# Kernel optimization log

Measured on AMD Instinct MI355X. Metric: run time of the kernel, lower is better.

The kernel has to match this reference:

```python
import jax, jax.numpy as jnp
import numpy as np

BS, S = 8, 1024
D_MODEL, N_HEADS, D_K = 256, 8, 32
H_SHARED, H_SEL = 2, 2
N_DYN = N_HEADS - H_SHARED
D_FF = 1024
N_BLOCKS = 2
L = 3 * N_BLOCKS  # blocks_1 (N_BLOCKS layers) + blocks_2 (2*N_BLOCKS layers)
NEG = -1e9


def _layernorm(x, g, b):
    m = x.mean(-1, keepdims=True)
    v = ((x - m) ** 2).mean(-1, keepdims=True)
    return (x - m) * jax.lax.rsqrt(v + 1e-5) * g + b


def _layer(p, mask_val, query, values, q4router, apply_pos):
    (Wq, bq, Wv, bv, Wg, Wo, bo, g1, be1, Wf1, bf1, Wf2, bf2, g2, be2) = p
    bs, s, dm = query.shape
    q = query @ Wq + bq            # kq_same=True -> k = q
    v = values @ Wv + bv
    qh = q.reshape(bs, s, N_HEADS, D_K).transpose(0, 2, 1, 3)   # [b,h,s,d]
    vh = v.reshape(bs, s, N_HEADS, D_K).transpose(0, 2, 1, 3)
    scores = jnp.einsum('bhqd,bhkd->bhqk', qh, qh) / (D_K ** 0.5)
    # nopeek = triu(ones,k=mask); allowed where nopeek==0 -> col < row + mask
    allowed = jnp.arange(s)[None, :] < (jnp.arange(s)[:, None] + mask_val)
    scores = jnp.where(allowed[None, None], scores, NEG)
    attnw = jax.nn.softmax(scores, axis=-1)
    # head routing: replicate torch view->permute->reshape order exactly
    qr = q4router.reshape(bs, s, N_HEADS, D_K).transpose(0, 2, 1, 3).reshape(bs * s, N_HEADS * D_K)
    gates = jax.nn.softmax(qr @ Wg, axis=1)                     # [bs*s, N_DYN]
    _, idx = jax.lax.top_k(gates, H_SEL)
    dyn_mask = jax.nn.one_hot(idx, N_DYN, dtype=gates.dtype).sum(axis=1)
    dyn_scores = gates * dyn_mask
    hs = dyn_mask.sum(axis=0)
    hp = gates.mean(axis=0)
    bal = ((hs / (hs.sum() + 1e-5)) * (hp / (hp.sum() + 1e-5))).sum()
    routing = jnp.concatenate(
        [jnp.ones((bs, s, H_SHARED), gates.dtype), dyn_scores.reshape(bs, s, N_DYN)], axis=-1)
    routing = routing.mean(axis=1)[:, :, None, None]            # [b,h,1,1]
    out = jnp.einsum('bhqk,bhkd->bhqd', attnw, vh) * routing
    out = out.transpose(0, 2, 1, 3).reshape(bs, s, dm) @ Wo + bo
    query = _layernorm(query + out, g1, be1)
    if apply_pos:
        ff = jax.nn.relu(query @ Wf1 + bf1) @ Wf2 + bf2
        query = _layernorm(query + ff, g2, be2)
    return query, bal


def _forward(q_embed_data, qa_embed_data, Wq, bq, Wv, bv, Wg, Wo, bo,
             ln1_w, ln1_b, Wf1, bf1, Wf2, bf2, ln2_w, ln2_b):
    stacks = (Wq, bq, Wv, bv, Wg, Wo, bo, ln1_w, ln1_b, Wf1, bf1, Wf2, bf2, ln2_w, ln2_b)
    params = [tuple(a[i] for a in stacks) for i in range(L)]
    x, y = q_embed_data, qa_embed_data
    for i in range(N_BLOCKS):
        y, _ = _layer(params[i], 1, y, y, x, True)
    attn = jnp.zeros((), jnp.float32)
    li = N_BLOCKS
    for _ in range(N_BLOCKS):
        x, _ = _layer(params[li], 1, x, x, x, False)  # self-block, no FFN
        li += 1
        x, attn = _layer(params[li], 0, x, y, x, True)  # cross to y, strict causal
        li += 1
    return x, attn


def setup_inputs():
    key = jax.random.key(0)
    ks = jax.random.split(key, 10)
    w = lambda k, shp: (jax.random.normal(k, shp, jnp.float32) * 0.02)
    return {
        'q_embed_data': jax.random.normal(ks[0], (BS, S, D_MODEL), jnp.float32),
        'qa_embed_data': jax.random.normal(ks[1], (BS, S, D_MODEL), jnp.float32),
        'Wq': w(ks[2], (L, D_MODEL, D_MODEL)), 'bq': jnp.zeros((L, D_MODEL), jnp.float32),
        'Wv': w(ks[3], (L, D_MODEL, D_MODEL)), 'bv': jnp.zeros((L, D_MODEL), jnp.float32),
        'Wg': w(ks[4], (L, D_MODEL, N_DYN)),
        'Wo': w(ks[5], (L, D_MODEL, D_MODEL)), 'bo': jnp.zeros((L, D_MODEL), jnp.float32),
        'ln1_w': jnp.ones((L, D_MODEL), jnp.float32), 'ln1_b': jnp.zeros((L, D_MODEL), jnp.float32),
        'Wf1': w(ks[6], (L, D_MODEL, D_FF)), 'bf1': jnp.zeros((L, D_FF), jnp.float32),
        'Wf2': w(ks[7], (L, D_FF, D_MODEL)), 'bf2': jnp.zeros((L, D_MODEL), jnp.float32),
        'ln2_w': jnp.ones((L, D_MODEL), jnp.float32), 'ln2_b': jnp.zeros((L, D_MODEL), jnp.float32),
    }


def reference(q_embed_data, qa_embed_data, Wq, bq, Wv, bv, Wg, Wo, bo,
              ln1_w, ln1_b, Wf1, bf1, Wf2, bf2, ln2_w, ln2_b):
    return _forward(q_embed_data, qa_embed_data, Wq, bq, Wv, bv, Wg, Wo, bo,
                    ln1_w, ln1_b, Wf1, bf1, Wf2, bf2, ln2_w, ln2_b)
```

## Files before the change

kernel.cpp:

```cpp
#include <hip/hip_runtime.h>


constexpr int DMODEL = 256;
constexpr int SEQ    = 1024;
constexpr int BATCH  = 8;
constexpr int NHEADS = 8;
constexpr int DKDIM  = 32;
constexpr int NDYN_C = 6;
constexpr int NTOK_C = BATCH * SEQ;
constexpr int DFF_C  = 1024;

using frag_bf16 = __attribute__((ext_vector_type(8))) short;
using f32x4    = __attribute__((ext_vector_type(4))) float;
typedef unsigned short ushort_t;

__device__ __forceinline__ ushort_t f2bf(float f) {
  unsigned u = __float_as_uint(f);
  unsigned r = (u + 0x7fffu + ((u >> 16) & 1u)) >> 16;
  return (ushort_t)r;
}

__device__ __forceinline__ unsigned cvt_pk_bf16(float lo, float hi) {
  unsigned r;
  asm("v_cvt_pk_bf16_f32 %0, %1, %2" : "=v"(r) : "v"(lo), "v"(hi));
  return r;
}

#define GLOAD_LDS16(gsrc, ldst)                                             \
  __builtin_amdgcn_global_load_lds(                                         \
      (const __attribute__((address_space(1))) void*)(gsrc),                \
      (__attribute__((address_space(3))) void*)(ldst), 16, 0, 0)

#define SYNC_DRAIN()                                                        \
  do {                                                                      \
    asm volatile("s_waitcnt vmcnt(0) lgkmcnt(0)" ::: "memory");             \
    __builtin_amdgcn_sched_barrier(0);                                      \
    __syncthreads();                                                        \
  } while (0)

template<int MODE>
__device__ __forceinline__
void gemm_body(int bx, int by,
               const ushort_t* __restrict__ A, const ushort_t* __restrict__ B,
               const float* __restrict__ bias, void* __restrict__ Cp,
               int M, int N, int K) {
  __shared__ ushort_t sA[2][4096];
  __shared__ ushort_t sB[2][4096];
  const int tid = threadIdx.x;
  const int wid = tid >> 6, lane = tid & 63;
  const int li = lane & 15, g = lane >> 4;
  const int wr = wid >> 1, wc = wid & 1;
  const int m0 = by * 64, n0 = bx * 64;
  f32x4 acc[2][2] = {};
  const int srow = wid * 8 + (lane >> 3);
  const int schk = (lane & 7) ^ (lane >> 3);
  const ushort_t* gA1 = &A[(size_t)(m0 + srow) * K + schk * 8];
  const ushort_t* gA2 = &A[(size_t)(m0 + 32 + srow) * K + schk * 8];
  const ushort_t* gB1 = &B[(size_t)(n0 + srow) * K + schk * 8];
  const ushort_t* gB2 = &B[(size_t)(n0 + 32 + srow) * K + schk * 8];
  const int nk = K >> 6;

  GLOAD_LDS16(gA1, sA[0] + wid * 512);
  GLOAD_LDS16(gA2, sA[0] + 2048 + wid * 512);
  GLOAD_LDS16(gB1, sB[0] + wid * 512);
  GLOAD_LDS16(gB2, sB[0] + 2048 + wid * 512);
  SYNC_DRAIN();

  auto compute = [&](int cur) {
#pragma unroll
    for (int s = 0; s < 2; ++s) {
      frag_bf16 af[2], bf[2];
#pragma unroll
      for (int m = 0; m < 2; ++m) {
        const int row = wr * 32 + m * 16 + li;
        af[m] = *reinterpret_cast<const frag_bf16*>(
            &sA[cur][row * 64 + ((s * 4 + g) ^ (row & 7)) * 8]);
      }
#pragma unroll
      for (int n = 0; n < 2; ++n) {
        const int row = wc * 32 + n * 16 + li;
        bf[n] = *reinterpret_cast<const frag_bf16*>(
            &sB[cur][row * 64 + ((s * 4 + g) ^ (row & 7)) * 8]);
      }
#pragma unroll
      for (int m = 0; m < 2; ++m)
#pragma unroll
        for (int n = 0; n < 2; ++n)
          acc[m][n] = __builtin_amdgcn_mfma_f32_16x16x32_bf16(af[m], bf[n], acc[m][n], 0, 0, 0);
    }
  };

  for (int kt = 0; kt < nk - 1; ++kt) {
    const int cur = kt & 1;
    const int k1 = (kt + 1) << 6;
    GLOAD_LDS16(gA1 + k1, sA[cur ^ 1] + wid * 512);
    GLOAD_LDS16(gA2 + k1, sA[cur ^ 1] + 2048 + wid * 512);
    GLOAD_LDS16(gB1 + k1, sB[cur ^ 1] + wid * 512);
    GLOAD_LDS16(gB2 + k1, sB[cur ^ 1] + 2048 + wid * 512);
    compute(cur);
    SYNC_DRAIN();
  }
  compute((nk - 1) & 1);

  constexpr float QSCALE = 0.42044820762685725f;
#pragma unroll
  for (int m = 0; m < 2; ++m)
#pragma unroll
    for (int n = 0; n < 2; ++n)
#pragma unroll
      for (int r = 0; r < 4; ++r) {
        const int mg = m0 + wr * 32 + m * 16 + g * 4 + r;
        const int ng = n0 + wc * 32 + n * 16 + li;
        if (MODE == 0) {
          ((float*)Cp)[(size_t)mg * N + ng] = acc[m][n][r] + bias[ng];
        } else if (MODE == 1) {
          ((ushort_t*)Cp)[(size_t)mg * N + ng] = f2bf((acc[m][n][r] + bias[ng]) * QSCALE);
        } else if (MODE == 2) {
          ((ushort_t*)Cp)[(size_t)mg * N + ng] = f2bf(fmaxf(acc[m][n][r] + bias[ng], 0.0f));
        } else {
          ((ushort_t*)Cp)[((size_t)((ng >> 10) * 256 + mg)) * SEQ + (ng & 1023)] =
              f2bf(acc[m][n][r] + bias[mg]);
        }
      }
}

template<int MODE>
__global__ __launch_bounds__(256)
void gemm_mfma_k(const ushort_t* __restrict__ A, const ushort_t* __restrict__ B,
                 const float* __restrict__ bias, void* __restrict__ Cp,
                 int M, int N, int K) {
  gemm_body<MODE>(blockIdx.x, blockIdx.y, A, B, bias, Cp, M, N, K);
}

__global__ __launch_bounds__(256)
void gemm_qv_k(const ushort_t* __restrict__ Aq, const ushort_t* __restrict__ Bq,
               const float* __restrict__ biasq, void* __restrict__ Cq,
               const ushort_t* __restrict__ Av, const ushort_t* __restrict__ Bv,
               const float* __restrict__ biasv, void* __restrict__ Cv) {
  if (blockIdx.z == 0)
    gemm_body<1>(blockIdx.y, blockIdx.x, Aq, Bq, biasq, Cq, NTOK_C, DMODEL, DMODEL);
  else
    gemm_body<3>(blockIdx.x, blockIdx.y, Av, Bv, biasv, Cv, DMODEL, NTOK_C, DMODEL);
}

__global__ __launch_bounds__(256)
void transpose_k(const float* __restrict__ in, ushort_t* __restrict__ out, int R, int C) {
  __shared__ float t[32][33];
  const int z = blockIdx.z;
  const int c0 = blockIdx.x * 32, r0 = blockIdx.y * 32;
  const int tx = threadIdx.x & 31, ty = threadIdx.x >> 5;
  const float* ip = in + (size_t)z * R * C;
  ushort_t* op = out + (size_t)z * R * C;
#pragma unroll
  for (int i = 0; i < 4; ++i) t[ty + 8 * i][tx] = ip[(size_t)(r0 + ty + 8 * i) * C + c0 + tx];
  __syncthreads();
#pragma unroll
  for (int i = 0; i < 4; ++i)
    op[(size_t)(c0 + ty + 8 * i) * R + r0 + tx] = f2bf(t[tx][ty + 8 * i]);
}

__global__ __launch_bounds__(256)
void conv_init_k(const float* __restrict__ src, float* __restrict__ dstF,
                 ushort_t* __restrict__ dstB) {
  const int i = blockIdx.x * 256 + threadIdx.x;
  const float4 v = reinterpret_cast<const float4*>(src)[i];
  reinterpret_cast<float4*>(dstF)[i] = v;
  ushort4 b;
  b.x = f2bf(v.x); b.y = f2bf(v.y); b.z = f2bf(v.z); b.w = f2bf(v.w);
  reinterpret_cast<ushort4*>(dstB)[i] = b;
}

__global__ __launch_bounds__(256)
void attn_mfma_k(const ushort_t* __restrict__ qb, const ushort_t* __restrict__ vbT,
                 const float* __restrict__ routing8, ushort_t* __restrict__ out,
                 int mask_val) {
  __shared__ ushort_t sk[2][2048];
  __shared__ ushort_t sv[2][2048];
  __shared__ ushort_t pbuf[4096];
  const int gid = blockIdx.x;
  const int b = gid & 7;
  const int slot = gid >> 3;
  const int h = (slot >> 4) & 7;
  const int qblk = 15 - (slot & 15);
  const int q0 = qblk * 64;
  const int tid = threadIdx.x;
  const int wave = tid >> 6, lane = tid & 63;
  const int g = lane >> 4, li = lane & 15;
  const int qw = q0 + wave * 16;
  const int qrow = qw + li;

  const frag_bf16 qf = *reinterpret_cast<const frag_bf16*>(
      &qb[((size_t)(b * SEQ + qrow)) * DMODEL + h * DKDIM + g * 8]);

  float mrun = -INFINITY, lrun = 0.f;
  f32x4 o0 = {0.f, 0.f, 0.f, 0.f}, o1 = {0.f, 0.f, 0.f, 0.f};
  ushort_t* pP = &pbuf[wave * 1024];

  const ushort_t* gK = &qb[((size_t)(b * SEQ + wave * 16 + li)) * DMODEL + h * DKDIM + g * 8];
  const ushort_t* gV = &vbT[((size_t)((b * NHEADS + h) * DKDIM) + wave * 8 + (lane >> 3)) * SEQ
                            + ((lane & 7) ^ (lane >> 3)) * 8];

  const int nt = qblk + 1;
  GLOAD_LDS16(gK, sk[0] + wave * 512);
  GLOAD_LDS16(gV, sv[0] + wave * 512);
  SYNC_DRAIN();

  auto tile_step = [&](int t, int cur) {
    const int kt = t * 64;
    f32x4 s[4];
#pragma unroll
    for (int kb = 0; kb < 4; ++kb) {
      frag_bf16 kf = *reinterpret_cast<const frag_bf16*>(&sk[cur][(kb * 64 + g * 16 + li) * 8]);
      f32x4 z = {0.f, 0.f, 0.f, 0.f};
      s[kb] = __builtin_amdgcn_mfma_f32_16x16x32_bf16(kf, qf, z, 0, 0, 0);
    }
    const bool need_mask = (kt + 63) >= (qw + mask_val);
    if (need_mask) {
#pragma unroll
      for (int kb = 0; kb < 4; ++kb)
#pragma unroll
        for (int r = 0; r < 4; ++r) {
          const int col = kt + kb * 16 + 4 * g + r;
          if (col >= (qrow + mask_val)) s[kb][r] = -1e9f;
        }
    }
    float tm = -INFINITY;
#pragma unroll
    for (int kb = 0; kb < 4; ++kb)
#pragma unroll
      for (int r = 0; r < 4; ++r) tm = fmaxf(tm, s[kb][r]);
    tm = fmaxf(tm, __shfl_xor(tm, 16, 64));
    tm = fmaxf(tm, __shfl_xor(tm, 32, 64));
    const float mnew = fmaxf(mrun, tm);
    const float scl = __expf(mrun - mnew);
    float p[4][4];
    float psum = 0.f;
#pragma unroll
    for (int kb = 0; kb < 4; ++kb)
#pragma unroll
      for (int r = 0; r < 4; ++r) { p[kb][r] = __expf(s[kb][r] - mnew); psum += p[kb][r]; }
    psum += __shfl_xor(psum, 16, 64);
    psum += __shfl_xor(psum, 32, 64);
    lrun = lrun * scl + psum;
    mrun = mnew;
#pragma unroll
    for (int r = 0; r < 4; ++r) { o0[r] *= scl; o1[r] *= scl; }
#pragma unroll
    for (int kb = 0; kb < 4; ++kb)
#pragma unroll
      for (int pair = 0; pair < 2; ++pair) {
        const unsigned pk = cvt_pk_bf16(p[kb][2 * pair], p[kb][2 * pair + 1]);
        const int addr = (((kb >> 1) * 4 + (kb & 1) * 2 + (g >> 1)) * 16 + li) * 8
                         + 4 * (g & 1) + 2 * pair;
        *reinterpret_cast<unsigned*>(&pP[addr]) = pk;
      }
    __threadfence_block();
#pragma unroll
    for (int c = 0; c < 2; ++c) {
      frag_bf16 pf = *reinterpret_cast<const frag_bf16*>(&pP[((c * 4 + g) * 16 + li) * 8]);
      frag_bf16 vf0 = *reinterpret_cast<const frag_bf16*>(
          &sv[cur][li * 64 + ((4 * c + g) ^ (li & 7)) * 8]);
      frag_bf16 vf1 = *reinterpret_cast<const frag_bf16*>(
          &sv[cur][(16 + li) * 64 + ((4 * c + g) ^ (li & 7)) * 8]);
      o0 = __builtin_amdgcn_mfma_f32_16x16x32_bf16(vf0, pf, o0, 0, 0, 0);
      o1 = __builtin_amdgcn_mfma_f32_16x16x32_bf16(vf1, pf, o1, 0, 0, 0);
    }
  };

  for (int t = 0; t < nt - 1; ++t) {
    const int cur = t & 1;
    const int kt = t * 64;
    GLOAD_LDS16(gK + (size_t)(kt + 64) * DMODEL, sk[cur ^ 1] + wave * 512);
    GLOAD_LDS16(gV + (kt + 64), sv[cur ^ 1] + wave * 512);
    tile_step(t, cur);
    SYNC_DRAIN();
  }
  tile_step(nt - 1, (nt - 1) & 1);

  const float rt = routing8[b * NHEADS + h];
  const float mult = rt / lrun;
  if (!(mask_val == 0 && qrow == 0)) {
    const size_t base = (size_t)(b * SEQ + qrow) * DMODEL + h * DKDIM;
    ushort4 w0, w1;
    w0.x = f2bf(o0[0] * mult); w0.y = f2bf(o0[1] * mult);
    w0.z = f2bf(o0[2] * mult); w0.w = f2bf(o0[3] * mult);
    w1.x = f2bf(o1[0] * mult); w1.y = f2bf(o1[1] * mult);
    w1.z = f2bf(o1[2] * mult); w1.w = f2bf(o1[3] * mult);
    *reinterpret_cast<ushort4*>(&out[base + 4 * g]) = w0;
    *reinterpret_cast<ushort4*>(&out[base + 16 + 4 * g]) = w1;
  }
  if (mask_val == 0 && qblk == 0 && wave == 0) {
    const int d = lane >> 1, hf = lane & 1;
    const ushort_t* src = &vbT[(((size_t)(b * NHEADS + h)) * DKDIM + d) * SEQ + hf * 512];
    float s = 0.f;
    for (int k = 0; k < 512; k += 8) {
      frag_bf16 v = *reinterpret_cast<const frag_bf16*>(&src[k]);
#pragma unroll
      for (int j = 0; j < 8; ++j)
        s += __uint_as_float(((unsigned)(ushort_t)v[j]) << 16);
    }
    s += __shfl_xor(s, 1, 64);
    if (hf == 0)
      out[(size_t)(b * SEQ) * DMODEL + h * DKDIM + d] = f2bf(s * (1.0f / 1024.0f) * rt);
  }
}

__global__ __launch_bounds__(128)
void router_k(const float* __restrict__ R, const float* __restrict__ Wg,
              float* __restrict__ partials) {
  __shared__ float sW[DMODEL * NDYN_C];
  __shared__ float red[18][128];
  const int tid = threadIdx.x;
  for (int t = tid; t < DMODEL * NDYN_C; t += 128) sW[t] = Wg[t];
  __syncthreads();
  const int r = blockIdx.x * 128 + tid;
  const int b = r >> 10;
  const int h = (r >> 7) & 7;
  const int s8 = r & 127;
  float lg[NDYN_C] = {};
  for (int t8 = 0; t8 < 8; ++t8) {
    const float* base = &R[((size_t)(b * SEQ + s8 * 8 + t8)) * DMODEL + h * DKDIM];
#pragma unroll
    for (int d = 0; d < DKDIM; ++d) {
      const float x = base[d];
      const float* w = &sW[(t8 * 32 + d) * NDYN_C];
#pragma unroll
      for (int j = 0; j < NDYN_C; ++j) lg[j] = fmaf(x, w[j], lg[j]);
    }
  }
  float mx = lg[0];
#pragma unroll
  for (int j = 1; j < NDYN_C; ++j) mx = fmaxf(mx, lg[j]);
  float e[NDYN_C], sum = 0.0f;
#pragma unroll
  for (int j = 0; j < NDYN_C; ++j) { e[j] = expf(lg[j] - mx); sum += e[j]; }
  float g[NDYN_C];
#pragma unroll
  for (int j = 0; j < NDYN_C; ++j) g[j] = e[j] / sum;
  int j1 = 0;
#pragma unroll
  for (int j = 1; j < NDYN_C; ++j) if (g[j] > g[j1]) j1 = j;
  int j2 = -1;
#pragma unroll
  for (int j = 0; j < NDYN_C; ++j) {
    if (j == j1) continue;
    if (j2 < 0 || g[j] > g[j2]) j2 = j;
  }
#pragma unroll
  for (int j = 0; j < NDYN_C; ++j) {
    const bool sel = (j == j1) || (j == j2);
    red[j][tid] = sel ? g[j] : 0.0f;
    red[6 + j][tid] = sel ? 1.0f : 0.0f;
    red[12 + j][tid] = g[j];
  }
  __syncthreads();
  if (tid < 18) {
    float s = 0.0f;
    for (int i = 0; i < 128; ++i) s += red[tid][i];
    partials[blockIdx.x * 18 + tid] = s;
  }
}

__global__ void router_reduce_k(const float* __restrict__ partials,
                                float* __restrict__ routing8,
                                float* __restrict__ bal_out) {
  const int tid = threadIdx.x;
  if (tid < 48) {
    const int b = tid / 6, j = tid % 6;
    float s = 0.0f;
    for (int t = 0; t < 8; ++t) s += partials[(b * 8 + t) * 18 + j];
    routing8[b * NHEADS + 2 + j] = s * (1.0f / 1024.0f);
  } else if (tid < 56) {
    const int b = tid - 48;
    routing8[b * NHEADS + 0] = 1.0f;
    routing8[b * NHEADS + 1] = 1.0f;
  } else if (tid == 56) {
    float hs[6], hp[6];
    float hssum = 0.0f, hpsum = 0.0f;
    for (int j = 0; j < 6; ++j) {
      float a = 0.0f, c = 0.0f;
      for (int bi = 0; bi < 64; ++bi) {
        a += partials[bi * 18 + 6 + j];
        c += partials[bi * 18 + 12 + j];
      }
      hs[j] = a;
      hp[j] = c * (1.0f / 8192.0f);
      hssum += hs[j];
      hpsum += hp[j];
    }
    float bal = 0.0f;
    for (int j = 0; j < 6; ++j)
      bal += (hs[j] / (hssum + 1e-5f)) * (hp[j] / (hpsum + 1e-5f));
    *bal_out = bal;
  }
}

__global__ __launch_bounds__(256)
void add_ln_k(const float* __restrict__ Xin, float* __restrict__ Xout,
              ushort_t* __restrict__ Xbf, const float* __restrict__ Y,
              const float* __restrict__ g, const float* __restrict__ be) {
  const int wave = threadIdx.x >> 6, lane = threadIdx.x & 63;
  const int r = blockIdx.x * 4 + wave;
  const size_t base = (size_t)r * DMODEL + lane * 4;
  float4 x = *reinterpret_cast<const float4*>(&Xin[base]);
  const float4 y = *reinterpret_cast<const float4*>(&Y[base]);
  x.x += y.x; x.y += y.y; x.z += y.z; x.w += y.w;
  float s = x.x + x.y + x.z + x.w;
#pragma unroll
  for (int o = 32; o >= 1; o >>= 1) s += __shfl_xor(s, o, 64);
  const float mean = s * (1.0f / DMODEL);
  const float4 d = {x.x - mean, x.y - mean, x.z - mean, x.w - mean};
  float v = d.x * d.x + d.y * d.y + d.z * d.z + d.w * d.w;
#pragma unroll
  for (int o = 32; o >= 1; o >>= 1) v += __shfl_xor(v, o, 64);
  const float rstd = 1.0f / sqrtf(v * (1.0f / DMODEL) + 1e-5f);
  const float4 gg = *reinterpret_cast<const float4*>(&g[lane * 4]);
  const float4 bb = *reinterpret_cast<const float4*>(&be[lane * 4]);
  float4 rv;
  rv.x = d.x * rstd * gg.x + bb.x;
  rv.y = d.y * rstd * gg.y + bb.y;
  rv.z = d.z * rstd * gg.z + bb.z;
  rv.w = d.w * rstd * gg.w + bb.w;
  *reinterpret_cast<float4*>(&Xout[base]) = rv;
  ushort4 o4;
  o4.x = f2bf(rv.x); o4.y = f2bf(rv.y); o4.z = f2bf(rv.z); o4.w = f2bf(rv.w);
  *reinterpret_cast<ushort4*>(&Xbf[base]) = o4;
}

extern "C" void kernel_launch(void* const* d_in, const int* in_sizes, int n_in,
                              void* d_out, int out_size, void* d_ws, size_t ws_size,
                              hipStream_t stream) {
  const float* q_embed  = (const float*)d_in[0];
  const float* qa_embed = (const float*)d_in[1];
  const float* Wq  = (const float*)d_in[2];
  const float* bq  = (const float*)d_in[3];
  const float* Wv  = (const float*)d_in[4];
  const float* bv  = (const float*)d_in[5];
  const float* Wg  = (const float*)d_in[6];
  const float* Wo  = (const float*)d_in[7];
  const float* bo  = (const float*)d_in[8];
  const float* ln1w = (const float*)d_in[9];
  const float* ln1b = (const float*)d_in[10];
  const float* Wf1 = (const float*)d_in[11];
  const float* bf1 = (const float*)d_in[12];
  const float* Wf2 = (const float*)d_in[13];
  const float* bf2 = (const float*)d_in[14];
  const float* ln2w = (const float*)d_in[15];
  const float* ln2b = (const float*)d_in[16];
  float* out = (float*)d_out;

  const size_t NA = (size_t)NTOK_C * DMODEL;
  float* xbuf = (float*)d_ws;
  float* ybuf = xbuf + NA;
  float* ob   = ybuf + NA;
  float* routing8   = ob + NA;
  float* partials   = routing8 + 64;
  float* balscratch = partials + 64 * 18;
  ushort_t* xbf   = (ushort_t*)(balscratch + 16);
  ushort_t* ybf   = xbf + NA;
  ushort_t* qb_bf = ybf + NA;
  ushort_t* vbT   = qb_bf + NA;
  ushort_t* ab_bf = vbT + NA;
  ushort_t* hb    = ab_bf + NA;
  ushort_t* WqT   = hb + (size_t)NTOK_C * DFF_C;
  ushort_t* WvT   = WqT + (size_t)6 * DMODEL * DMODEL;
  ushort_t* WoT   = WvT + (size_t)6 * DMODEL * DMODEL;
  ushort_t* Wf1T  = WoT + (size_t)6 * DMODEL * DMODEL;
  ushort_t* Wf2T  = Wf1T + (size_t)6 * DMODEL * DFF_C;

  transpose_k<<<dim3(8, 8, 6), 256, 0, stream>>>(Wq, WqT, DMODEL, DMODEL);
  transpose_k<<<dim3(8, 8, 6), 256, 0, stream>>>(Wv, WvT, DMODEL, DMODEL);
  transpose_k<<<dim3(8, 8, 6), 256, 0, stream>>>(Wo, WoT, DMODEL, DMODEL);
  transpose_k<<<dim3(32, 8, 6), 256, 0, stream>>>(Wf1, Wf1T, DMODEL, DFF_C);
  transpose_k<<<dim3(8, 32, 6), 256, 0, stream>>>(Wf2, Wf2T, DFF_C, DMODEL);
  conv_init_k<<<NA / 1024, 256, 0, stream>>>(q_embed, xbuf, xbf);
  conv_init_k<<<NA / 1024, 256, 0, stream>>>(qa_embed, ybuf, ybf);

  auto run_layer = [&](int l, float* Q, ushort_t* Qbf, const ushort_t* Vbf,
                       int mask_val, bool ffn, bool last) {
    const float* bq_l = bq + (size_t)l * DMODEL;
    const float* bv_l = bv + (size_t)l * DMODEL;
    const float* Wg_l = Wg + (size_t)l * DMODEL * NDYN_C;
    const float* bo_l = bo + (size_t)l * DMODEL;
    const float* g1_l = ln1w + (size_t)l * DMODEL;
    const float* b1_l = ln1b + (size_t)l * DMODEL;
    const ushort_t* WqT_l = WqT + (size_t)l * DMODEL * DMODEL;
    const ushort_t* WvT_l = WvT + (size_t)l * DMODEL * DMODEL;
    const ushort_t* WoT_l = WoT + (size_t)l * DMODEL * DMODEL;

    router_k<<<64, 128, 0, stream>>>(xbuf, Wg_l, partials);
    router_reduce_k<<<1, 64, 0, stream>>>(partials, routing8,
                                          last ? (out + NA) : balscratch);
    gemm_qv_k<<<dim3(128, 4, 2), 256, 0, stream>>>(
        Qbf, WqT_l, bq_l, qb_bf, WvT_l, Vbf, bv_l, vbT);
    attn_mfma_k<<<1024, 256, 0, stream>>>(qb_bf, vbT, routing8, ab_bf, mask_val);
    gemm_mfma_k<0><<<dim3(4, 128), 256, 0, stream>>>(
        ab_bf, WoT_l, bo_l, ob, NTOK_C, DMODEL, DMODEL);
    add_ln_k<<<NTOK_C / 4, 256, 0, stream>>>(Q, Q, Qbf, ob, g1_l, b1_l);
    if (ffn) {
      const float* bf1_l = bf1 + (size_t)l * DFF_C;
      const float* bf2_l = bf2 + (size_t)l * DMODEL;
      const float* g2_l = ln2w + (size_t)l * DMODEL;
      const float* b2_l = ln2b + (size_t)l * DMODEL;
      const ushort_t* Wf1T_l = Wf1T + (size_t)l * DMODEL * DFF_C;
      const ushort_t* Wf2T_l = Wf2T + (size_t)l * DFF_C * DMODEL;
      gemm_mfma_k<2><<<dim3(16, 128), 256, 0, stream>>>(
          Qbf, Wf1T_l, bf1_l, hb, NTOK_C, DFF_C, DMODEL);
      gemm_mfma_k<0><<<dim3(4, 128), 256, 0, stream>>>(
          hb, Wf2T_l, bf2_l, ob, NTOK_C, DMODEL, DFF_C);
      add_ln_k<<<NTOK_C / 4, 256, 0, stream>>>(Q, last ? out : Q, Qbf, ob, g2_l, b2_l);
    }
  };

  run_layer(0, ybuf, ybf, ybf, 1, true, false);
  run_layer(1, ybuf, ybf, ybf, 1, true, false);
  run_layer(2, xbuf, xbf, xbf, 1, false, false);
  run_layer(3, xbuf, xbf, ybf, 0, true, false);
  run_layer(4, xbuf, xbf, xbf, 1, false, false);
  run_layer(5, xbuf, xbf, ybf, 0, true, true);
}
```

Measured before the change: 587.2 us.

## Fuse router into QV GEMM launch and merge setup kernels to cut launches

The per-layer router kernel becomes extra blocks of the Q/V projection GEMM launch, and the attention kernel reduces the routing partials itself, so router_reduce only runs on the last layer. The three square weight transposes and the two embedding conversions are each merged into single launches. GEMM mode changes from a template parameter to a runtime argument, which adds branches to the epilogue. The aim is fewer kernel launches and less serialization, at the cost of runtime mode checks and each attention block re-reading the partials.

Measured after the change: 547.1 us. -6.8%, faster.

```diff
diff --git a/kernel.cpp b/kernel.cpp
--- a/kernel.cpp
+++ b/kernel.cpp
@@ -38,14 +38,12 @@
     __syncthreads();                                                        \
   } while (0)
 
-template<int MODE>
 __device__ __forceinline__
-void gemm_body(int bx, int by,
+void gemm_body(int mode, int bx, int by,
                const ushort_t* __restrict__ A, const ushort_t* __restrict__ B,
                const float* __restrict__ bias, void* __restrict__ Cp,
-               int M, int N, int K) {
-  __shared__ ushort_t sA[2][4096];
-  __shared__ ushort_t sB[2][4096];
+               int M, int N, int K,
+               ushort_t (*sA)[4096], ushort_t (*sB)[4096]) {
   const int tid = threadIdx.x;
   const int wid = tid >> 6, lane = tid & 63;
   const int li = lane & 15, g = lane >> 4;
@@ -111,11 +109,11 @@
       for (int r = 0; r < 4; ++r) {
         const int mg = m0 + wr * 32 + m * 16 + g * 4 + r;
         const int ng = n0 + wc * 32 + n * 16 + li;
-        if (MODE == 0) {
+        if (mode == 0) {
           ((float*)Cp)[(size_t)mg * N + ng] = acc[m][n][r] + bias[ng];
-        } else if (MODE == 1) {
+        } else if (mode == 1) {
           ((ushort_t*)Cp)[(size_t)mg * N + ng] = f2bf((acc[m][n][r] + bias[ng]) * QSCALE);
-        } else if (MODE == 2) {
+        } else if (mode == 2) {
           ((ushort_t*)Cp)[(size_t)mg * N + ng] = f2bf(fmaxf(acc[m][n][r] + bias[ng], 0.0f));
         } else {
           ((ushort_t*)Cp)[((size_t)((ng >> 10) * 256 + mg)) * SEQ + (ng & 1023)] =
@@ -124,33 +122,99 @@
       }
 }
 
-template<int MODE>
-__global__ __launch_bounds__(256)
-void gemm_mfma_k(const ushort_t* __restrict__ A, const ushort_t* __restrict__ B,
+__global__ __launch_bounds__(256)
+void gemm_mfma_k(int mode, const ushort_t* __restrict__ A, const ushort_t* __restrict__ B,
                  const float* __restrict__ bias, void* __restrict__ Cp,
                  int M, int N, int K) {
-  gemm_body<MODE>(blockIdx.x, blockIdx.y, A, B, bias, Cp, M, N, K);
-}
-
-__global__ __launch_bounds__(256)
-void gemm_qv_k(const ushort_t* __restrict__ Aq, const ushort_t* __restrict__ Bq,
-               const float* __restrict__ biasq, void* __restrict__ Cq,
-               const ushort_t* __restrict__ Av, const ushort_t* __restrict__ Bv,
-               const float* __restrict__ biasv, void* __restrict__ Cv) {
+  __shared__ ushort_t sA[2][4096];
+  __shared__ ushort_t sB[2][4096];
+  gemm_body(mode, blockIdx.x, blockIdx.y, A, B, bias, Cp, M, N, K, sA, sB);
+}
+
+__device__ __forceinline__
+void router_body(const float* __restrict__ R, const float* __restrict__ Wg,
+                 float* __restrict__ partials, float* sW, float (*red)[128]) {
+  const int tid = threadIdx.x;
+  for (int t = tid; t < DMODEL * NDYN_C; t += 256) sW[t] = Wg[t];
+  __syncthreads();
+  if (tid < 128) {
+    const int r = blockIdx.x * 128 + tid;
+    const int b = r >> 10;
+    const int h = (r >> 7) & 7;
+    const int s8 = r & 127;
+    float lg[NDYN_C] = {};
+    for (int t8 = 0; t8 < 8; ++t8) {
+      const float* base = &R[((size_t)(b * SEQ + s8 * 8 + t8)) * DMODEL + h * DKDIM];
+#pragma unroll
+      for (int d = 0; d < DKDIM; ++d) {
+        const float x = base[d];
+        const float* w = &sW[(t8 * 32 + d) * NDYN_C];
+#pragma unroll
+        for (int j = 0; j < NDYN_C; ++j) lg[j] = fmaf(x, w[j], lg[j]);
+      }
+    }
+    float mx = lg[0];
+#pragma unroll
+    for (int j = 1; j < NDYN_C; ++j) mx = fmaxf(mx, lg[j]);
+    float e[NDYN_C], sum = 0.0f;
+#pragma unroll
+    for (int j = 0; j < NDYN_C; ++j) { e[j] = expf(lg[j] - mx); sum += e[j]; }
+    float g[NDYN_C];
+#pragma unroll
+    for (int j = 0; j < NDYN_C; ++j) g[j] = e[j] / sum;
+    int j1 = 0;
+#pragma unroll
+    for (int j = 1; j < NDYN_C; ++j) if (g[j] > g[j1]) j1 = j;
+    int j2 = -1;
+#pragma unroll
+    for (int j = 0; j < NDYN_C; ++j) {
+      if (j == j1) continue;
+      if (j2 < 0 || g[j] > g[j2]) j2 = j;
+    }
+#pragma unroll
+    for (int j = 0; j < NDYN_C; ++j) {
+      const bool sel = (j == j1) || (j == j2);
+      red[j][tid] = sel ? g[j] : 0.0f;
+      red[6 + j][tid] = sel ? 1.0f : 0.0f;
+      red[12 + j][tid] = g[j];
+    }
+  }
+  __syncthreads();
+  if (tid < 18) {
+    float s = 0.0f;
+    for (int i = 0; i < 128; ++i) s += red[tid][i];
+    partials[blockIdx.x * 18 + tid] = s;
+  }
+}
+
+__global__ __launch_bounds__(256)
+void gemm_qv_router_k(const ushort_t* __restrict__ Aq, const ushort_t* __restrict__ Bq,
+                      const float* __restrict__ biasq, void* __restrict__ Cq,
+                      const ushort_t* __restrict__ Av, const ushort_t* __restrict__ Bv,
+                      const float* __restrict__ biasv, void* __restrict__ Cv,
+                      const float* __restrict__ R, const float* __restrict__ Wg,
+                      float* __restrict__ partials) {
+  __shared__ ushort_t sA[2][4096];
+  __shared__ ushort_t sB[2][4096];
+  if (blockIdx.y == 4) {
+    if (blockIdx.z == 0 && blockIdx.x < 64) {
+      float* sW = (float*)&sA[0][0];
+      float (*red)[128] = (float(*)[128])&sB[0][0];
+      router_body(R, Wg, partials, sW, red);
+    }
+    return;
+  }
   if (blockIdx.z == 0)
-    gemm_body<1>(blockIdx.y, blockIdx.x, Aq, Bq, biasq, Cq, NTOK_C, DMODEL, DMODEL);
+    gemm_body(1, blockIdx.y, blockIdx.x, Aq, Bq, biasq, Cq, NTOK_C, DMODEL, DMODEL, sA, sB);
   else
-    gemm_body<3>(blockIdx.x, blockIdx.y, Av, Bv, biasv, Cv, DMODEL, NTOK_C, DMODEL);
-}
-
-__global__ __launch_bounds__(256)
-void transpose_k(const float* __restrict__ in, ushort_t* __restrict__ out, int R, int C) {
+    gemm_body(3, blockIdx.x, blockIdx.y, Av, Bv, biasv, Cv, DMODEL, NTOK_C, DMODEL, sA, sB);
+}
+
+__device__ __forceinline__
+void transpose_body(const float* __restrict__ ip, ushort_t* __restrict__ op, int R, int C,
+                    int c0, int r0) {
   __shared__ float t[32][33];
-  const int z = blockIdx.z;
-  const int c0 = blockIdx.x * 32, r0 = blockIdx.y * 32;
   const int tx = threadIdx.x & 31, ty = threadIdx.x >> 5;
-  const float* ip = in + (size_t)z * R * C;
-  ushort_t* op = out + (size_t)z * R * C;
 #pragma unroll
   for (int i = 0; i < 4; ++i) t[ty + 8 * i][tx] = ip[(size_t)(r0 + ty + 8 * i) * C + c0 + tx];
   __syncthreads();
@@ -160,8 +224,32 @@
 }
 
 __global__ __launch_bounds__(256)
-void conv_init_k(const float* __restrict__ src, float* __restrict__ dstF,
-                 ushort_t* __restrict__ dstB) {
+void transpose_k(const float* __restrict__ in, ushort_t* __restrict__ out, int R, int C) {
+  const int z = blockIdx.z;
+  transpose_body(in + (size_t)z * R * C, out + (size_t)z * R * C, R, C,
+                 blockIdx.x * 32, blockIdx.y * 32);
+}
+
+__global__ __launch_bounds__(256)
+void transpose3_k(const float* __restrict__ W0, ushort_t* __restrict__ O0,
+                  const float* __restrict__ W1, ushort_t* __restrict__ O1,
+                  const float* __restrict__ W2, ushort_t* __restrict__ O2) {
+  const int z = blockIdx.z;
+  const int zi = z / 6, zz = z % 6;
+  const float* in = (zi == 0) ? W0 : (zi == 1) ? W1 : W2;
+  ushort_t* out = (zi == 0) ? O0 : (zi == 1) ? O1 : O2;
+  transpose_body(in + (size_t)zz * DMODEL * DMODEL, out + (size_t)zz * DMODEL * DMODEL,
+                 DMODEL, DMODEL, blockIdx.x * 32, blockIdx.y * 32);
+}
+
+__global__ __launch_bounds__(256)
+void conv_init_k(const float* __restrict__ s0, float* __restrict__ f0,
+                 ushort_t* __restrict__ b0,
+                 const float* __restrict__ s1, float* __restrict__ f1,
+                 ushort_t* __restrict__ b1) {
+  const float* src = blockIdx.y ? s1 : s0;
+  float* dstF = blockIdx.y ? f1 : f0;
+  ushort_t* dstB = blockIdx.y ? b1 : b0;
   const int i = blockIdx.x * 256 + threadIdx.x;
   const float4 v = reinterpret_cast<const float4*>(src)[i];
   reinterpret_cast<float4*>(dstF)[i] = v;
@@ -172,7 +260,7 @@
 
 __global__ __launch_bounds__(256)
 void attn_mfma_k(const ushort_t* __restrict__ qb, const ushort_t* __restrict__ vbT,
-                 const float* __restrict__ routing8, ushort_t* __restrict__ out,
+                 const float* __restrict__ partials, ushort_t* __restrict__ out,
                  int mask_val) {
   __shared__ ushort_t sk[2][2048];
   __shared__ ushort_t sv[2][2048];
@@ -277,7 +365,14 @@
   }
   tile_step(nt - 1, (nt - 1) & 1);
 
-  const float rt = routing8[b * NHEADS + h];
+  float rt = 1.0f;
+  if (h >= 2) {
+    const int j = h - 2;
+    float sr = 0.f;
+#pragma unroll
+    for (int t = 0; t < 8; ++t) sr += partials[(b * 8 + t) * 18 + j];
+    rt = sr * (1.0f / 1024.0f);
+  }
   const float mult = rt / lrun;
   if (!(mask_val == 0 && qrow == 0)) {
     const size_t base = (size_t)(b * SEQ + qrow) * DMODEL + h * DKDIM;
@@ -305,76 +400,10 @@
   }
 }
 
-__global__ __launch_bounds__(128)
-void router_k(const float* __restrict__ R, const float* __restrict__ Wg,
-              float* __restrict__ partials) {
-  __shared__ float sW[DMODEL * NDYN_C];
-  __shared__ float red[18][128];
-  const int tid = threadIdx.x;
-  for (int t = tid; t < DMODEL * NDYN_C; t += 128) sW[t] = Wg[t];
-  __syncthreads();
-  const int r = blockIdx.x * 128 + tid;
-  const int b = r >> 10;
-  const int h = (r >> 7) & 7;
-  const int s8 = r & 127;
-  float lg[NDYN_C] = {};
-  for (int t8 = 0; t8 < 8; ++t8) {
-    const float* base = &R[((size_t)(b * SEQ + s8 * 8 + t8)) * DMODEL + h * DKDIM];
-#pragma unroll
-    for (int d = 0; d < DKDIM; ++d) {
-      const float x = base[d];
-      const float* w = &sW[(t8 * 32 + d) * NDYN_C];
-#pragma unroll
-      for (int j = 0; j < NDYN_C; ++j) lg[j] = fmaf(x, w[j], lg[j]);
-    }
-  }
-  float mx = lg[0];
-#pragma unroll
-  for (int j = 1; j < NDYN_C; ++j) mx = fmaxf(mx, lg[j]);
-  float e[NDYN_C], sum = 0.0f;
-#pragma unroll
-  for (int j = 0; j < NDYN_C; ++j) { e[j] = expf(lg[j] - mx); sum += e[j]; }
-  float g[NDYN_C];
-#pragma unroll
-  for (int j = 0; j < NDYN_C; ++j) g[j] = e[j] / sum;
-  int j1 = 0;
-#pragma unroll
-  for (int j = 1; j < NDYN_C; ++j) if (g[j] > g[j1]) j1 = j;
-  int j2 = -1;
-#pragma unroll
-  for (int j = 0; j < NDYN_C; ++j) {
-    if (j == j1) continue;
-    if (j2 < 0 || g[j] > g[j2]) j2 = j;
-  }
-#pragma unroll
-  for (int j = 0; j < NDYN_C; ++j) {
-    const bool sel = (j == j1) || (j == j2);
-    red[j][tid] = sel ? g[j] : 0.0f;
-    red[6 + j][tid] = sel ? 1.0f : 0.0f;
-    red[12 + j][tid] = g[j];
-  }
-  __syncthreads();
-  if (tid < 18) {
-    float s = 0.0f;
-    for (int i = 0; i < 128; ++i) s += red[tid][i];
-    partials[blockIdx.x * 18 + tid] = s;
-  }
-}
-
 __global__ void router_reduce_k(const float* __restrict__ partials,
-                                float* __restrict__ routing8,
                                 float* __restrict__ bal_out) {
   const int tid = threadIdx.x;
-  if (tid < 48) {
-    const int b = tid / 6, j = tid % 6;
-    float s = 0.0f;
-    for (int t = 0; t < 8; ++t) s += partials[(b * 8 + t) * 18 + j];
-    routing8[b * NHEADS + 2 + j] = s * (1.0f / 1024.0f);
-  } else if (tid < 56) {
-    const int b = tid - 48;
-    routing8[b * NHEADS + 0] = 1.0f;
-    routing8[b * NHEADS + 1] = 1.0f;
-  } else if (tid == 56) {
+  if (tid == 0) {
     float hs[6], hp[6];
     float hssum = 0.0f, hpsum = 0.0f;
     for (int j = 0; j < 6; ++j) {
@@ -468,13 +497,11 @@
   ushort_t* Wf1T  = WoT + (size_t)6 * DMODEL * DMODEL;
   ushort_t* Wf2T  = Wf1T + (size_t)6 * DMODEL * DFF_C;
 
-  transpose_k<<<dim3(8, 8, 6), 256, 0, stream>>>(Wq, WqT, DMODEL, DMODEL);
-  transpose_k<<<dim3(8, 8, 6), 256, 0, stream>>>(Wv, WvT, DMODEL, DMODEL);
-  transpose_k<<<dim3(8, 8, 6), 256, 0, stream>>>(Wo, WoT, DMODEL, DMODEL);
+  transpose3_k<<<dim3(8, 8, 18), 256, 0, stream>>>(Wq, WqT, Wv, WvT, Wo, WoT);
   transpose_k<<<dim3(32, 8, 6), 256, 0, stream>>>(Wf1, Wf1T, DMODEL, DFF_C);
   transpose_k<<<dim3(8, 32, 6), 256, 0, stream>>>(Wf2, Wf2T, DFF_C, DMODEL);
-  conv_init_k<<<NA / 1024, 256, 0, stream>>>(q_embed, xbuf, xbf);
-  conv_init_k<<<NA / 1024, 256, 0, stream>>>(qa_embed, ybuf, ybf);
+  conv_init_k<<<dim3(NA / 1024, 2), 256, 0, stream>>>(q_embed, xbuf, xbf,
+                                                      qa_embed, ybuf, ybf);
 
   auto run_layer = [&](int l, float* Q, ushort_t* Qbf, const ushort_t* Vbf,
                        int mask_val, bool ffn, bool last) {
@@ -488,14 +515,13 @@
     const ushort_t* WvT_l = WvT + (size_t)l * DMODEL * DMODEL;
     const ushort_t* WoT_l = WoT + (size_t)l * DMODEL * DMODEL;
 
-    router_k<<<64, 128, 0, stream>>>(xbuf, Wg_l, partials);
-    router_reduce_k<<<1, 64, 0, stream>>>(partials, routing8,
-                                          last ? (out + NA) : balscratch);
-    gemm_qv_k<<<dim3(128, 4, 2), 256, 0, stream>>>(
-        Qbf, WqT_l, bq_l, qb_bf, WvT_l, Vbf, bv_l, vbT);
-    attn_mfma_k<<<1024, 256, 0, stream>>>(qb_bf, vbT, routing8, ab_bf, mask_val);
-    gemm_mfma_k<0><<<dim3(4, 128), 256, 0, stream>>>(
-        ab_bf, WoT_l, bo_l, ob, NTOK_C, DMODEL, DMODEL);
+    gemm_qv_router_k<<<dim3(128, 5, 2), 256, 0, stream>>>(
+        Qbf, WqT_l, bq_l, qb_bf, WvT_l, Vbf, bv_l, vbT, xbuf, Wg_l, partials);
+    if (last)
+      router_reduce_k<<<1, 64, 0, stream>>>(partials, out + NA);
+    attn_mfma_k<<<1024, 256, 0, stream>>>(qb_bf, vbT, partials, ab_bf, mask_val);
+    gemm_mfma_k<<<dim3(4, 128), 256, 0, stream>>>(
+        0, ab_bf, WoT_l, bo_l, ob, NTOK_C, DMODEL, DMODEL);
     add_ln_k<<<NTOK_C / 4, 256, 0, stream>>>(Q, Q, Qbf, ob, g1_l, b1_l);
     if (ffn) {
       const float* bf1_l = bf1 + (size_t)l * DFF_C;
@@ -504,10 +530,10 @@
       const float* b2_l = ln2b + (size_t)l * DMODEL;
       const ushort_t* Wf1T_l = Wf1T + (size_t)l * DMODEL * DFF_C;
       const ushort_t* Wf2T_l = Wf2T + (size_t)l * DFF_C * DMODEL;
-      gemm_mfma_k<2><<<dim3(16, 128), 256, 0, stream>>>(
-          Qbf, Wf1T_l, bf1_l, hb, NTOK_C, DFF_C, DMODEL);
-      gemm_mfma_k<0><<<dim3(4, 128), 256, 0, stream>>>(
-          hb, Wf2T_l, bf2_l, ob, NTOK_C, DMODEL, DFF_C);
+      gemm_mfma_k<<<dim3(16, 128), 256, 0, stream>>>(
+          2, Qbf, Wf1T_l, bf1_l, hb, NTOK_C, DFF_C, DMODEL);
+      gemm_mfma_k<<<dim3(4, 128), 256, 0, stream>>>(
+          0, hb, Wf2T_l, bf2_l, ob, NTOK_C, DMODEL, DFF_C);
       add_ln_k<<<NTOK_C / 4, 256, 0, stream>>>(Q, last ? out : Q, Qbf, ob, g2_l, b2_l);
     }
   };
```
